# Kernel tuning notes

Measured on AMD Instinct MI355X. Metric: run time of the kernel, lower is better.

Reference implementation:

```python
import jax, jax.numpy as jnp
from jax import lax
import numpy as np

H = 64  # hidden_dim


def _lstm_dir(x, W_ih, W_hh, b, reverse):
    # x: [B,T,I]; W_ih: [4H,I]; W_hh: [4H,H]; b: [4H] (b_ih+b_hh combined)
    B = x.shape[0]
    xp = jnp.einsum('bti,gi->btg', x, W_ih) + b          # [B,T,4H]
    xp = jnp.swapaxes(xp, 0, 1)                          # [T,B,4H]

    def step(carry, xt):
        h, c = carry
        g = xt + h @ W_hh.T                              # [B,4H]
        i, f, gg, o = jnp.split(g, 4, axis=-1)           # PyTorch gate order i,f,g,o
        i = jax.nn.sigmoid(i)
        f = jax.nn.sigmoid(f)
        gg = jnp.tanh(gg)
        o = jax.nn.sigmoid(o)
        c = f * c + i * gg
        h = o * jnp.tanh(c)
        return (h, c), h

    init = (jnp.zeros((B, H), x.dtype), jnp.zeros((B, H), x.dtype))
    _, hs = lax.scan(step, init, xp, reverse=reverse)    # outputs aligned to original positions
    return jnp.swapaxes(hs, 0, 1)                        # [B,T,H]


def _bilstm_layer(x, Wih_f, Whh_f, b_f, Wih_b, Whh_b, b_b):
    fwd = _lstm_dir(x, Wih_f, Whh_f, b_f, reverse=False)
    bwd = _lstm_dir(x, Wih_b, Whh_b, b_b, reverse=True)
    return jnp.concatenate([fwd, bwd], axis=-1)          # [B,T,2H]


def setup_inputs() -> dict:
    key = jax.random.key(0)
    ks = jax.random.split(key, 16)
    s = 0.1
    d = {}
    d['x'] = jax.random.normal(ks[0], (512, 512, 4), dtype=jnp.float32)
    # layer 0 (input size 4), forward / backward directions
    d['Wih_l0_f'] = jax.random.normal(ks[1], (4 * H, 4)) * s
    d['Whh_l0_f'] = jax.random.normal(ks[2], (4 * H, H)) * s
    d['b_l0_f'] = jax.random.normal(ks[3], (4 * H,)) * s
    d['Wih_l0_b'] = jax.random.normal(ks[4], (4 * H, 4)) * s
    d['Whh_l0_b'] = jax.random.normal(ks[5], (4 * H, H)) * s
    d['b_l0_b'] = jax.random.normal(ks[6], (4 * H,)) * s
    # layer 1 (input size 2H = 128)
    d['Wih_l1_f'] = jax.random.normal(ks[7], (4 * H, 2 * H)) * s
    d['Whh_l1_f'] = jax.random.normal(ks[8], (4 * H, H)) * s
    d['b_l1_f'] = jax.random.normal(ks[9], (4 * H,)) * s
    d['Wih_l1_b'] = jax.random.normal(ks[10], (4 * H, 2 * H)) * s
    d['Whh_l1_b'] = jax.random.normal(ks[11], (4 * H, H)) * s
    d['b_l1_b'] = jax.random.normal(ks[12], (4 * H,)) * s
    # final linear: 2H -> 1
    d['fc_w'] = jax.random.normal(ks[13], (1, 2 * H)) * s
    d['fc_b'] = jax.random.normal(ks[14], (1,)) * s
    return d


def reference(x, Wih_l0_f, Whh_l0_f, b_l0_f, Wih_l0_b, Whh_l0_b, b_l0_b,
              Wih_l1_f, Whh_l1_f, b_l1_f, Wih_l1_b, Whh_l1_b, b_l1_b,
              fc_w, fc_b):
    h0 = _bilstm_layer(x, Wih_l0_f, Whh_l0_f, b_l0_f, Wih_l0_b, Whh_l0_b, b_l0_b)
    h1 = _bilstm_layer(h0, Wih_l1_f, Whh_l1_f, b_l1_f, Wih_l1_b, Whh_l1_b, b_l1_b)
    pooled = jnp.mean(h1, axis=1)                        # [B,2H]
    return pooled @ fc_w.T + fc_b                        # [B,1]
```

## Files before the change

kernel.cpp:

```cpp
#include <hip/hip_runtime.h>

#define H  64
#define TT 512
#define BB 512
#define CSTR 80
#define UCH 16
#define XSTRF 260

typedef _Float16 half8 __attribute__((ext_vector_type(8)));
typedef float    f32x4 __attribute__((ext_vector_type(4)));

__device__ __forceinline__ float frcp(float x) { return __builtin_amdgcn_rcpf(x); }
__device__ __forceinline__ float sigm(float x) { return frcp(1.f + __expf(-x)); }
__device__ __forceinline__ float tanh_fast(float x) { return 1.f - 2.f * frcp(__expf(2.f * x) + 1.f); }

__global__ __launch_bounds__(256) void xpad_prep(const float* __restrict__ x,
                                                 _Float16* __restrict__ xpad) {
    int gid = blockIdx.x * 256 + threadIdx.x;
    int row = gid >> 2, q = gid & 3;
    half8 v = {0,0,0,0,0,0,0,0};
    if (q == 0) {
        float4 xv = ((const float4*)x)[row];
        v[0] = (_Float16)xv.x; v[1] = (_Float16)xv.y;
        v[2] = (_Float16)xv.z; v[3] = (_Float16)xv.w;
    }
    *(half8*)(xpad + (size_t)row * 32 + q * 8) = v;
}

__global__ __launch_bounds__(256, 2) void lstm_l0(
    const _Float16* __restrict__ xpad,
    const float* __restrict__ WihF, const float* __restrict__ WhhF, const float* __restrict__ bF,
    const float* __restrict__ WihB, const float* __restrict__ WhhB, const float* __restrict__ bB,
    _Float16* __restrict__ out0)
{
    const int dir = blockIdx.x & 1;
    const int b0  = (blockIdx.x >> 1) * 2;
    const int tid = threadIdx.x;
    const int w = tid >> 6, l = tid & 63, m = l & 15, q = l >> 4;
    const int ch  = m & 1;
    const int ubo = (m >> 1) & 3;
    const int uo  = w * 16 + ubo * 4 + q;
    const bool act = (m < 8);

    const float* Wih = dir ? WihB : WihF;
    const float* Whh = dir ? WhhB : WhhF;
    const float* bia = dir ? bB   : bF;

    half8 Ah[4][2];
#pragma unroll
    for (int ub = 0; ub < 4; ++ub) {
        const int wrow = (m & 3) * 64 + (w * 16 + ub * 4 + (m >> 2));
#pragma unroll
        for (int s2 = 0; s2 < 2; ++s2) {
            const float* src = Whh + wrow * 64 + s2 * 32 + q * 8;
            half8 tmp;
#pragma unroll
            for (int j = 0; j < 8; ++j) tmp[j] = (_Float16)src[j];
            Ah[ub][s2] = tmp;
        }
    }

    half8 Bg[4];
    float bvj[4];
#pragma unroll
    for (int j = 0; j < 4; ++j) {
        const int n  = w * 64 + j * 16 + m;
        const int gr = (n & 3) * 64 + (n >> 2);
        bvj[j] = bia[gr];
        half8 tmp;
#pragma unroll
        for (int jj = 0; jj < 8; ++jj) {
            int k = q * 8 + jj;
            tmp[jj] = (k < 4) ? (_Float16)Wih[gr * 4 + k] : (_Float16)0.f;
        }
        Bg[j] = tmp;
    }

    __shared__ __align__(16) float xp[2][UCH][XSTRF];
    __shared__ _Float16 hbuf[2][2][CSTR];
    for (int i = tid; i < 2 * 2 * CSTR / 2; i += 256) ((unsigned int*)hbuf)[i] = 0u;
    __syncthreads();

    float c = 0.f;
    int p = 0;

    for (int chunk = 0; chunk < TT / UCH; ++chunk) {
        const int c0 = chunk * UCH;

#pragma unroll
        for (int cc = 0; cc < 2; ++cc) {
            const int tA = dir ? (TT - 1 - (c0 + m)) : (c0 + m);
            half8 a0 = *(const half8*)(xpad + (size_t)((b0 + cc) * TT + tA) * 32 + q * 8);
#pragma unroll
            for (int j = 0; j < 4; ++j) {
                f32x4 acc = {bvj[j], bvj[j], bvj[j], bvj[j]};
                acc = __builtin_amdgcn_mfma_f32_16x16x32_f16(a0, Bg[j], acc, 0, 0, 0);
#pragma unroll
                for (int i = 0; i < 4; ++i)
                    xp[cc][q * 4 + i][w * 64 + j * 16 + m] = acc[i];
            }
        }

        f32x4 xv = *(const f32x4*)&xp[ch][0][uo * 4];
        for (int u = 0; u < UCH; ++u) {
            int un = (u + 1 < UCH) ? (u + 1) : u;
            f32x4 xn = *(const f32x4*)&xp[ch][un][uo * 4];

            half8 ah0 = *(const half8*)&hbuf[p][ch][q * 8];
            half8 ah1 = *(const half8*)&hbuf[p][ch][32 + q * 8];

            f32x4 g_own;
#pragma unroll
            for (int ub = 0; ub < 4; ++ub) {
                f32x4 a = __builtin_amdgcn_mfma_f32_16x16x32_f16(Ah[ub][0], ah0, xv, 0, 0, 0);
                a       = __builtin_amdgcn_mfma_f32_16x16x32_f16(Ah[ub][1], ah1, a, 0, 0, 0);
                if (ub == ubo) g_own = a;
            }

            float e_i = sigm(g_own[0]), e_f = sigm(g_own[1]);
            float e_g = tanh_fast(g_own[2]), e_o = sigm(g_own[3]);
            c = e_f * c + e_i * e_g;
            float hh = e_o * tanh_fast(c);

            if (act) {
                const int tg = dir ? (TT - 1 - (c0 + u)) : (c0 + u);
                out0[((size_t)(b0 + ch) * TT + tg) * 128 + dir * 64 + uo] = (_Float16)hh;
                hbuf[p ^ 1][ch][uo] = (_Float16)hh;
            }
            __syncthreads();
            p ^= 1; xv = xn;
        }
    }
}

__global__ __launch_bounds__(256, 2) void lstm_l1(
    const _Float16* __restrict__ out0,
    const float* __restrict__ WihF, const float* __restrict__ WhhF, const float* __restrict__ bF,
    const float* __restrict__ WihB, const float* __restrict__ WhhB, const float* __restrict__ bB,
    float* __restrict__ pooled)
{
    const int dir = blockIdx.x & 1;
    const int b0  = (blockIdx.x >> 1) * 2;
    const int tid = threadIdx.x;
    const int w = tid >> 6, l = tid & 63, m = l & 15, q = l >> 4;
    const int ch  = m & 1;
    const int ubo = (m >> 1) & 3;
    const int uo  = w * 16 + ubo * 4 + q;
    const bool act = (m < 8);

    const float* Wih = dir ? WihB : WihF;
    const float* Whh = dir ? WhhB : WhhF;
    const float* bia = dir ? bB   : bF;

    half8 Ah[4][2];
#pragma unroll
    for (int ub = 0; ub < 4; ++ub) {
        const int wrow = (m & 3) * 64 + (w * 16 + ub * 4 + (m >> 2));
#pragma unroll
        for (int s2 = 0; s2 < 2; ++s2) {
            const float* src = Whh + wrow * 64 + s2 * 32 + q * 8;
            half8 tmp;
#pragma unroll
            for (int j = 0; j < 8; ++j) tmp[j] = (_Float16)src[j];
            Ah[ub][s2] = tmp;
        }
    }

    half8 Bg[4][4];
    float bvj[4];
#pragma unroll
    for (int j = 0; j < 4; ++j) {
        const int n  = w * 64 + j * 16 + m;
        const int gr = (n & 3) * 64 + (n >> 2);
        bvj[j] = bia[gr];
#pragma unroll
        for (int k4 = 0; k4 < 4; ++k4) {
            const float* src = Wih + gr * 128 + k4 * 32 + q * 8;
            half8 tmp;
#pragma unroll
            for (int jj = 0; jj < 8; ++jj) tmp[jj] = (_Float16)src[jj];
            Bg[j][k4] = tmp;
        }
    }

    __shared__ __align__(16) float xp[2][UCH][XSTRF];
    __shared__ _Float16 hbuf[2][2][CSTR];
    for (int i = tid; i < 2 * 2 * CSTR / 2; i += 256) ((unsigned int*)hbuf)[i] = 0u;
    __syncthreads();

    float c = 0.f, hs = 0.f;
    int p = 0;

    for (int chunk = 0; chunk < TT / UCH; ++chunk) {
        const int c0 = chunk * UCH;

#pragma unroll
        for (int cc = 0; cc < 2; ++cc) {
            const int tA = dir ? (TT - 1 - (c0 + m)) : (c0 + m);
            const _Float16* arow = out0 + (size_t)((b0 + cc) * TT + tA) * 128 + q * 8;
            half8 a0 = *(const half8*)(arow);
            half8 a1 = *(const half8*)(arow + 32);
            half8 a2 = *(const half8*)(arow + 64);
            half8 a3 = *(const half8*)(arow + 96);
#pragma unroll
            for (int j = 0; j < 4; ++j) {
                f32x4 acc = {bvj[j], bvj[j], bvj[j], bvj[j]};
                acc = __builtin_amdgcn_mfma_f32_16x16x32_f16(a0, Bg[j][0], acc, 0, 0, 0);
                acc = __builtin_amdgcn_mfma_f32_16x16x32_f16(a1, Bg[j][1], acc, 0, 0, 0);
                acc = __builtin_amdgcn_mfma_f32_16x16x32_f16(a2, Bg[j][2], acc, 0, 0, 0);
                acc = __builtin_amdgcn_mfma_f32_16x16x32_f16(a3, Bg[j][3], acc, 0, 0, 0);
#pragma unroll
                for (int i = 0; i < 4; ++i)
                    xp[cc][q * 4 + i][w * 64 + j * 16 + m] = acc[i];
            }
        }

        f32x4 xv = *(const f32x4*)&xp[ch][0][uo * 4];
        for (int u = 0; u < UCH; ++u) {
            int un = (u + 1 < UCH) ? (u + 1) : u;
            f32x4 xn = *(const f32x4*)&xp[ch][un][uo * 4];

            half8 ah0 = *(const half8*)&hbuf[p][ch][q * 8];
            half8 ah1 = *(const half8*)&hbuf[p][ch][32 + q * 8];

            f32x4 g_own;
#pragma unroll
            for (int ub = 0; ub < 4; ++ub) {
                f32x4 a = __builtin_amdgcn_mfma_f32_16x16x32_f16(Ah[ub][0], ah0, xv, 0, 0, 0);
                a       = __builtin_amdgcn_mfma_f32_16x16x32_f16(Ah[ub][1], ah1, a, 0, 0, 0);
                if (ub == ubo) g_own = a;
            }

            float e_i = sigm(g_own[0]), e_f = sigm(g_own[1]);
            float e_g = tanh_fast(g_own[2]), e_o = sigm(g_own[3]);
            c = e_f * c + e_i * e_g;
            float hh = e_o * tanh_fast(c);
            hs += hh;

            if (act) hbuf[p ^ 1][ch][uo] = (_Float16)hh;
            __syncthreads();
            p ^= 1; xv = xn;
        }
    }

    if (act) pooled[(size_t)(b0 + ch) * 128 + dir * 64 + uo] = hs;
}

__global__ __launch_bounds__(64) void fc_head(
    const float* __restrict__ pooled,
    const float* __restrict__ fcw, const float* __restrict__ fcb,
    float* __restrict__ out)
{
    const int b = blockIdx.x;
    const int l = threadIdx.x;
    float v = pooled[b * 128 + l] * fcw[l] + pooled[b * 128 + 64 + l] * fcw[64 + l];
#pragma unroll
    for (int o = 32; o > 0; o >>= 1) v += __shfl_down(v, o);
    if (l == 0) out[b] = v * (1.f / (float)TT) + fcb[0];
}

extern "C" void kernel_launch(void* const* d_in, const int* in_sizes, int n_in,
                              void* d_out, int out_size, void* d_ws, size_t ws_size,
                              hipStream_t stream) {
    const float* x       = (const float*)d_in[0];
    const float* Wih_l0f = (const float*)d_in[1];
    const float* Whh_l0f = (const float*)d_in[2];
    const float* b_l0f   = (const float*)d_in[3];
    const float* Wih_l0b = (const float*)d_in[4];
    const float* Whh_l0b = (const float*)d_in[5];
    const float* b_l0b   = (const float*)d_in[6];
    const float* Wih_l1f = (const float*)d_in[7];
    const float* Whh_l1f = (const float*)d_in[8];
    const float* b_l1f   = (const float*)d_in[9];
    const float* Wih_l1b = (const float*)d_in[10];
    const float* Whh_l1b = (const float*)d_in[11];
    const float* b_l1b   = (const float*)d_in[12];
    const float* fcw     = (const float*)d_in[13];
    const float* fcb     = (const float*)d_in[14];

    const size_t o_xpad   = 0;
    const size_t o_out0   = o_xpad + (size_t)BB * TT * 32 * 2;
    const size_t o_pooled = o_out0 + (size_t)BB * TT * 128 * 2;

    _Float16* xpad   = (_Float16*)((char*)d_ws + o_xpad);
    _Float16* out0   = (_Float16*)((char*)d_ws + o_out0);
    float*    pooled = (float*)((char*)d_ws + o_pooled);

    xpad_prep<<<(BB * TT * 4) / 256, 256, 0, stream>>>(x, xpad);
    lstm_l0<<<(BB / 2) * 2, 256, 0, stream>>>(xpad, Wih_l0f, Whh_l0f, b_l0f,
                                              Wih_l0b, Whh_l0b, b_l0b, out0);
    lstm_l1<<<(BB / 2) * 2, 256, 0, stream>>>(out0, Wih_l1f, Whh_l1f, b_l1f,
                                              Wih_l1b, Whh_l1b, b_l1b, pooled);
    fc_head<<<BB, 64, 0, stream>>>(pooled, fcw, fcb, (float*)d_out);
}
```

Before: 482.7 us.

## Process four batch rows per LSTM block with prefetched inputs and a lighter barrier

Each recurrent block now handles four batch rows instead of two, so every lane of the 16x16 MFMA output holds a useful gate result, and the grid is halved to 256 blocks. Input rows for the next chunk are prefetched into registers during the current chunk. The per-step __syncthreads is replaced by an inline s_waitcnt lgkmcnt(0) plus s_barrier. The cost is fewer blocks (256 on a GPU with many CUs, occupancy hint lowered to 1), so latency hiding across blocks may drop, and the per-block LDS for the xp buffer doubles.

```diff
diff --git a/kernel.cpp b/kernel.cpp
--- a/kernel.cpp
+++ b/kernel.cpp
@@ -6,6 +6,7 @@
 #define CSTR 80
 #define UCH 16
 #define XSTRF 260
+#define NCHUNK (TT / UCH)
 
 typedef _Float16 half8 __attribute__((ext_vector_type(8)));
 typedef float    f32x4 __attribute__((ext_vector_type(4)));
@@ -13,6 +14,10 @@
 __device__ __forceinline__ float frcp(float x) { return __builtin_amdgcn_rcpf(x); }
 __device__ __forceinline__ float sigm(float x) { return frcp(1.f + __expf(-x)); }
 __device__ __forceinline__ float tanh_fast(float x) { return 1.f - 2.f * frcp(__expf(2.f * x) + 1.f); }
+
+__device__ __forceinline__ void step_barrier() {
+    asm volatile("s_waitcnt lgkmcnt(0)\n\ts_barrier" ::: "memory");
+}
 
 __global__ __launch_bounds__(256) void xpad_prep(const float* __restrict__ x,
                                                  _Float16* __restrict__ xpad) {
@@ -27,20 +32,19 @@
     *(half8*)(xpad + (size_t)row * 32 + q * 8) = v;
 }
 
-__global__ __launch_bounds__(256, 2) void lstm_l0(
+__global__ __launch_bounds__(256, 1) void lstm_l0(
     const _Float16* __restrict__ xpad,
     const float* __restrict__ WihF, const float* __restrict__ WhhF, const float* __restrict__ bF,
     const float* __restrict__ WihB, const float* __restrict__ WhhB, const float* __restrict__ bB,
     _Float16* __restrict__ out0)
 {
     const int dir = blockIdx.x & 1;
-    const int b0  = (blockIdx.x >> 1) * 2;
+    const int b0  = (blockIdx.x >> 1) * 4;
     const int tid = threadIdx.x;
     const int w = tid >> 6, l = tid & 63, m = l & 15, q = l >> 4;
-    const int ch  = m & 1;
-    const int ubo = (m >> 1) & 3;
+    const int ch  = m & 3;
+    const int ubo = m >> 2;
     const int uo  = w * 16 + ubo * 4 + q;
-    const bool act = (m < 8);
 
     const float* Wih = dir ? WihB : WihF;
     const float* Whh = dir ? WhhB : WhhF;
@@ -76,29 +80,42 @@
         Bg[j] = tmp;
     }
 
-    __shared__ __align__(16) float xp[2][UCH][XSTRF];
-    __shared__ _Float16 hbuf[2][2][CSTR];
-    for (int i = tid; i < 2 * 2 * CSTR / 2; i += 256) ((unsigned int*)hbuf)[i] = 0u;
+    __shared__ __align__(16) float xp[4][UCH][XSTRF];
+    __shared__ __align__(16) _Float16 hbuf[2][4][CSTR];
+    for (int i = tid; i < 2 * 4 * CSTR / 2; i += 256) ((unsigned int*)hbuf)[i] = 0u;
     __syncthreads();
 
     float c = 0.f;
     int p = 0;
 
-    for (int chunk = 0; chunk < TT / UCH; ++chunk) {
+    half8 a[4];
+    {
+        const int tA = dir ? (TT - 1 - m) : m;
+#pragma unroll
+        for (int cc = 0; cc < 4; ++cc)
+            a[cc] = *(const half8*)(xpad + (size_t)((b0 + cc) * TT + tA) * 32 + q * 8);
+    }
+
+    for (int chunk = 0; chunk < NCHUNK; ++chunk) {
         const int c0 = chunk * UCH;
 
 #pragma unroll
-        for (int cc = 0; cc < 2; ++cc) {
-            const int tA = dir ? (TT - 1 - (c0 + m)) : (c0 + m);
-            half8 a0 = *(const half8*)(xpad + (size_t)((b0 + cc) * TT + tA) * 32 + q * 8);
+        for (int cc = 0; cc < 4; ++cc) {
 #pragma unroll
             for (int j = 0; j < 4; ++j) {
                 f32x4 acc = {bvj[j], bvj[j], bvj[j], bvj[j]};
-                acc = __builtin_amdgcn_mfma_f32_16x16x32_f16(a0, Bg[j], acc, 0, 0, 0);
+                acc = __builtin_amdgcn_mfma_f32_16x16x32_f16(a[cc], Bg[j], acc, 0, 0, 0);
 #pragma unroll
                 for (int i = 0; i < 4; ++i)
                     xp[cc][q * 4 + i][w * 64 + j * 16 + m] = acc[i];
             }
+        }
+        if (chunk + 1 < NCHUNK) {
+            const int c0n = c0 + UCH;
+            const int tA = dir ? (TT - 1 - (c0n + m)) : (c0n + m);
+#pragma unroll
+            for (int cc = 0; cc < 4; ++cc)
+                a[cc] = *(const half8*)(xpad + (size_t)((b0 + cc) * TT + tA) * 32 + q * 8);
         }
 
         f32x4 xv = *(const f32x4*)&xp[ch][0][uo * 4];
@@ -112,9 +129,9 @@
             f32x4 g_own;
 #pragma unroll
             for (int ub = 0; ub < 4; ++ub) {
-                f32x4 a = __builtin_amdgcn_mfma_f32_16x16x32_f16(Ah[ub][0], ah0, xv, 0, 0, 0);
-                a       = __builtin_amdgcn_mfma_f32_16x16x32_f16(Ah[ub][1], ah1, a, 0, 0, 0);
-                if (ub == ubo) g_own = a;
+                f32x4 g = __builtin_amdgcn_mfma_f32_16x16x32_f16(Ah[ub][0], ah0, xv, 0, 0, 0);
+                g       = __builtin_amdgcn_mfma_f32_16x16x32_f16(Ah[ub][1], ah1, g, 0, 0, 0);
+                if (ub == ubo) g_own = g;
             }
 
             float e_i = sigm(g_own[0]), e_f = sigm(g_own[1]);
@@ -122,31 +139,28 @@
             c = e_f * c + e_i * e_g;
             float hh = e_o * tanh_fast(c);
 
-            if (act) {
-                const int tg = dir ? (TT - 1 - (c0 + u)) : (c0 + u);
-                out0[((size_t)(b0 + ch) * TT + tg) * 128 + dir * 64 + uo] = (_Float16)hh;
-                hbuf[p ^ 1][ch][uo] = (_Float16)hh;
-            }
-            __syncthreads();
+            const int tg = dir ? (TT - 1 - (c0 + u)) : (c0 + u);
+            out0[((size_t)(b0 + ch) * TT + tg) * 128 + dir * 64 + uo] = (_Float16)hh;
+            hbuf[p ^ 1][ch][uo] = (_Float16)hh;
+            step_barrier();
             p ^= 1; xv = xn;
         }
     }
 }
 
-__global__ __launch_bounds__(256, 2) void lstm_l1(
+__global__ __launch_bounds__(256, 1) void lstm_l1(
     const _Float16* __restrict__ out0,
     const float* __restrict__ WihF, const float* __restrict__ WhhF, const float* __restrict__ bF,
     const float* __restrict__ WihB, const float* __restrict__ WhhB, const float* __restrict__ bB,
     float* __restrict__ pooled)
 {
     const int dir = blockIdx.x & 1;
-    const int b0  = (blockIdx.x >> 1) * 2;
+    const int b0  = (blockIdx.x >> 1) * 4;
     const int tid = threadIdx.x;
     const int w = tid >> 6, l = tid & 63, m = l & 15, q = l >> 4;
-    const int ch  = m & 1;
-    const int ubo = (m >> 1) & 3;
+    const int ch  = m & 3;
+    const int ubo = m >> 2;
     const int uo  = w * 16 + ubo * 4 + q;
-    const bool act = (m < 8);
 
     const float* Wih = dir ? WihB : WihF;
     const float* Whh = dir ? WhhB : WhhF;
@@ -183,35 +197,52 @@
         }
     }
 
-    __shared__ __align__(16) float xp[2][UCH][XSTRF];
-    __shared__ _Float16 hbuf[2][2][CSTR];
-    for (int i = tid; i < 2 * 2 * CSTR / 2; i += 256) ((unsigned int*)hbuf)[i] = 0u;
+    __shared__ __align__(16) float xp[4][UCH][XSTRF];
+    __shared__ __align__(16) _Float16 hbuf[2][4][CSTR];
+    for (int i = tid; i < 2 * 4 * CSTR / 2; i += 256) ((unsigned int*)hbuf)[i] = 0u;
     __syncthreads();
 
     float c = 0.f, hs = 0.f;
     int p = 0;
 
-    for (int chunk = 0; chunk < TT / UCH; ++chunk) {
+    half8 a[4][4];
+    {
+        const int tA = dir ? (TT - 1 - m) : m;
+#pragma unroll
+        for (int cc = 0; cc < 4; ++cc) {
+            const _Float16* arow = out0 + (size_t)((b0 + cc) * TT + tA) * 128 + q * 8;
+#pragma unroll
+            for (int k4 = 0; k4 < 4; ++k4)
+                a[cc][k4] = *(const half8*)(arow + k4 * 32);
+        }
+    }
+
+    for (int chunk = 0; chunk < NCHUNK; ++chunk) {
         const int c0 = chunk * UCH;
 
 #pragma unroll
-        for (int cc = 0; cc < 2; ++cc) {
-            const int tA = dir ? (TT - 1 - (c0 + m)) : (c0 + m);
-            const _Float16* arow = out0 + (size_t)((b0 + cc) * TT + tA) * 128 + q * 8;
-            half8 a0 = *(const half8*)(arow);
-            half8 a1 = *(const half8*)(arow + 32);
-            half8 a2 = *(const half8*)(arow + 64);
-            half8 a3 = *(const half8*)(arow + 96);
+        for (int cc = 0; cc < 4; ++cc) {
 #pragma unroll
             for (int j = 0; j < 4; ++j) {
                 f32x4 acc = {bvj[j], bvj[j], bvj[j], bvj[j]};
-                acc = __builtin_amdgcn_mfma_f32_16x16x32_f16(a0, Bg[j][0], acc, 0, 0, 0);
-                acc = __builtin_amdgcn_mfma_f32_16x16x32_f16(a1, Bg[j][1], acc, 0, 0, 0);
-                acc = __builtin_amdgcn_mfma_f32_16x16x32_f16(a2, Bg[j][2], acc, 0, 0, 0);
-                acc = __builtin_amdgcn_mfma_f32_16x16x32_f16(a3, Bg[j][3], acc, 0, 0, 0);
+                acc = __builtin_amdgcn_mfma_f32_16x16x32_f16(a[cc][0], Bg[j][0], acc, 0, 0, 0);
+                acc = __builtin_amdgcn_mfma_f32_16x16x32_f16(a[cc][1], Bg[j][1], acc, 0, 0, 0);
+                acc = __builtin_amdgcn_mfma_f32_16x16x32_f16(a[cc][2], Bg[j][2], acc, 0, 0, 0);
+                acc = __builtin_amdgcn_mfma_f32_16x16x32_f16(a[cc][3], Bg[j][3], acc, 0, 0, 0);
 #pragma unroll
                 for (int i = 0; i < 4; ++i)
                     xp[cc][q * 4 + i][w * 64 + j * 16 + m] = acc[i];
+            }
+        }
+        if (chunk + 1 < NCHUNK) {
+            const int c0n = c0 + UCH;
+            const int tA = dir ? (TT - 1 - (c0n + m)) : (c0n + m);
+#pragma unroll
+            for (int cc = 0; cc < 4; ++cc) {
+                const _Float16* arow = out0 + (size_t)((b0 + cc) * TT + tA) * 128 + q * 8;
+#pragma unroll
+                for (int k4 = 0; k4 < 4; ++k4)
+                    a[cc][k4] = *(const half8*)(arow + k4 * 32);
             }
         }
 
@@ -226,9 +257,9 @@
             f32x4 g_own;
 #pragma unroll
             for (int ub = 0; ub < 4; ++ub) {
-                f32x4 a = __builtin_amdgcn_mfma_f32_16x16x32_f16(Ah[ub][0], ah0, xv, 0, 0, 0);
-                a       = __builtin_amdgcn_mfma_f32_16x16x32_f16(Ah[ub][1], ah1, a, 0, 0, 0);
-                if (ub == ubo) g_own = a;
+                f32x4 g = __builtin_amdgcn_mfma_f32_16x16x32_f16(Ah[ub][0], ah0, xv, 0, 0, 0);
+                g       = __builtin_amdgcn_mfma_f32_16x16x32_f16(Ah[ub][1], ah1, g, 0, 0, 0);
+                if (ub == ubo) g_own = g;
             }
 
             float e_i = sigm(g_own[0]), e_f = sigm(g_own[1]);
@@ -237,13 +268,13 @@
             float hh = e_o * tanh_fast(c);
             hs += hh;
 
-            if (act) hbuf[p ^ 1][ch][uo] = (_Float16)hh;
-            __syncthreads();
+            hbuf[p ^ 1][ch][uo] = (_Float16)hh;
+            step_barrier();
             p ^= 1; xv = xn;
         }
     }
 
-    if (act) pooled[(size_t)(b0 + ch) * 128 + dir * 64 + uo] = hs;
+    pooled[(size_t)(b0 + ch) * 128 + dir * 64 + uo] = hs;
 }
 
 __global__ __launch_bounds__(64) void fc_head(
@@ -287,9 +318,9 @@
     float*    pooled = (float*)((char*)d_ws + o_pooled);
 
     xpad_prep<<<(BB * TT * 4) / 256, 256, 0, stream>>>(x, xpad);
-    lstm_l0<<<(BB / 2) * 2, 256, 0, stream>>>(xpad, Wih_l0f, Whh_l0f, b_l0f,
+    lstm_l0<<<(BB / 4) * 2, 256, 0, stream>>>(xpad, Wih_l0f, Whh_l0f, b_l0f,
                                               Wih_l0b, Whh_l0b, b_l0b, out0);
-    lstm_l1<<<(BB / 2) * 2, 256, 0, stream>>>(out0, Wih_l1f, Whh_l1f, b_l1f,
+    lstm_l1<<<(BB / 4) * 2, 256, 0, stream>>>(out0, Wih_l1f, Whh_l1f, b_l1f,
                                               Wih_l1b, Whh_l1b, b_l1b, pooled);
     fc_head<<<BB, 64, 0, stream>>>(pooled, fcw, fcb, (float*)d_out);
 }
```

Result: faster. 450.8 us (-6.6%).
